# Optimization experiments

Measured on AMD Instinct MI355X. Metric: run time of the kernel, lower is better.

## Reference

```python
import jax, jax.numpy as jnp
import numpy as np

B, T, N, E = 32, 512, 4, 16          # batch, seq_len, num_nodes, num_edges (N*N)
NI, EI = 16, 8                        # node / edge input channels
HN, HE, MH, C = 128, 128, 256, 8      # hidden node/edge, mlp hidden, classes

# complete-graph edge list (matches the src/dst double loop in __init__)
SRC = np.repeat(np.arange(N), N)      # [E]
DST = np.tile(np.arange(N), N)        # [E]
# GCNConv (PyG default) adds self-loops on top of the existing complete graph
# -> adjacency counts: off-diag 1, diag 2; in-degree of every node = N+1.
# symmetric norm deg^-1/2 A deg^-1/2 collapses to A/(N+1). Dense 4x4 matmul
# per graph is the efficient faithful form of the scatter-add here.
NORM_ADJ = (np.ones((N, N), np.float32) + np.eye(N, dtype=np.float32)) / (N + 1)


def lstm(x, Wih, Whh, b):
    """batch_first LSTM, torch gate order (i,f,g,o). x: [Bn,T,D] -> [Bn,T,H]."""
    H = Whh.shape[0]
    xz = x @ Wih + b  # precompute input projection [Bn,T,4H]

    def step(carry, zt):
        h, c = carry
        z = zt + h @ Whh
        i, f, g, o = jnp.split(z, 4, axis=-1)
        c = jax.nn.sigmoid(f) * c + jax.nn.sigmoid(i) * jnp.tanh(g)
        h = jax.nn.sigmoid(o) * jnp.tanh(c)
        return (h, c), h

    init = (jnp.zeros((x.shape[0], H), x.dtype), jnp.zeros((x.shape[0], H), x.dtype))
    _, hs = jax.lax.scan(step, init, jnp.swapaxes(xz, 0, 1))
    return jnp.swapaxes(hs, 0, 1)


def setup_inputs() -> dict:
    key = jax.random.key(0)
    ks = jax.random.split(key, 30)

    def p(k, shape, s=0.05):
        return (jax.random.normal(k, shape, jnp.float32) * s)

    return {
        "x_seq": jax.random.normal(ks[0], (B, T, N, NI), jnp.float32),
        "edge_attr_seq": jax.random.normal(ks[1], (B, T, E, EI), jnp.float32),
        "Wn1": p(ks[2], (NI, HN)), "bn1": p(ks[3], (HN,)),
        "Wn2": p(ks[4], (HN, HN)), "bn2": p(ks[5], (HN,)),
        "We1": p(ks[6], (EI, HE)), "be1": p(ks[7], (HE,)),
        "We2": p(ks[8], (HE, HE)), "be2": p(ks[9], (HE,)),
        "Wg1": p(ks[10], (HN, HN)), "bg1": p(ks[11], (HN,)),
        "Wg2": p(ks[12], (HN, HN)), "bg2": p(ks[13], (HN,)),
        "Wef1": p(ks[14], (HE, HE)), "bef1": p(ks[15], (HE,)),
        "Wef2": p(ks[16], (HE, HE)), "bef2": p(ks[17], (HE,)),
        "Wih_n": p(ks[18], (HN, 4 * HN)), "Whh_n": p(ks[19], (HN, 4 * HN)), "b_n": p(ks[20], (4 * HN,)),
        "Wih_e": p(ks[21], (HE, 4 * HE)), "Whh_e": p(ks[22], (HE, 4 * HE)), "b_e": p(ks[23], (4 * HE,)),
        "Wc1": p(ks[24], (2 * HN + HE, MH)), "bc1": p(ks[25], (MH,)),
        "Wc2": p(ks[26], (MH, C)), "bc2": p(ks[27], (C,)),
    }


def reference(x_seq, edge_attr_seq, Wn1, bn1, Wn2, bn2, We1, be1, We2, be2,
              Wg1, bg1, Wg2, bg2, Wef1, bef1, Wef2, bef2,
              Wih_n, Whh_n, b_n, Wih_e, Whh_e, b_e, Wc1, bc1, Wc2, bc2):
    adj = jnp.asarray(NORM_ADJ)
    # node / edge MLP embeddings
    x = jax.nn.relu(jax.nn.relu(x_seq @ Wn1 + bn1) @ Wn2 + bn2)      # [B,T,N,HN]
    e = jax.nn.relu(jax.nn.relu(edge_attr_seq @ We1 + be1) @ We2 + be2)  # [B,T,E,HE]
    # two GCN layers: normalized-adjacency aggregation per (batch,time) graph
    x = jax.nn.relu(jnp.einsum('ij,btjd->btid', adj, x @ Wg1) + bg1)
    x = jax.nn.relu(jnp.einsum('ij,btjd->btid', adj, x @ Wg2) + bg2)
    # edge FC stack
    e = jax.nn.relu(jax.nn.relu(e @ Wef1 + bef1) @ Wef2 + bef2)
    # LSTMs over time, one sequence per (batch, node) / (batch, edge)
    xn = x.transpose(0, 2, 1, 3).reshape(B * N, T, HN)
    en = e.transpose(0, 2, 1, 3).reshape(B * E, T, HE)
    hn = lstm(xn, Wih_n, Whh_n, b_n).reshape(B, N, T, HN).transpose(0, 2, 1, 3)  # [B,T,N,HN]
    he = lstm(en, Wih_e, Whh_e, b_e).reshape(B, E, T, HE).transpose(0, 2, 1, 3)  # [B,T,E,HE]
    # edge-gather classifier
    src_f = hn[:, :, jnp.asarray(SRC), :]
    dst_f = hn[:, :, jnp.asarray(DST), :]
    feats = jnp.concatenate([src_f, dst_f, he], axis=-1)  # [B,T,E,2HN+HE]
    logits = jax.nn.relu(feats @ Wc1 + bc1) @ Wc2 + bc2   # [B,T,E,C]
    return logits
```

## Files before the change

kernel.cpp:

```cpp
#include <hip/hip_runtime.h>
#include <cstdint>

constexpr int T_  = 512;
constexpr int HN_ = 128;

#define DEVI __device__ __forceinline__

typedef __bf16 bf16x8 __attribute__((ext_vector_type(8)));
typedef __bf16 bf16x4 __attribute__((ext_vector_type(4)));
typedef __bf16 bf16x2 __attribute__((ext_vector_type(2)));
typedef float  f32x4  __attribute__((ext_vector_type(4)));

DEVI float sigf(float x) { return __builtin_amdgcn_rcpf(1.f + __expf(-x)); }
DEVI float tanh_fast(float x) {
  x = fminf(fmaxf(x, -15.f), 15.f);
  return 1.f - 2.f * __builtin_amdgcn_rcpf(1.f + __expf(2.f * x));
}

DEVI void layer128_bf(const __bf16* __restrict__ src, __bf16* __restrict__ dst,
                      bf16x8 w0, bf16x8 w1, bf16x8 w2, bf16x8 w3,
                      float bv, int lm, int lh, int n)
{
  #pragma unroll
  for (int m = 0; m < 4; ++m) {
    const __bf16* sp = &src[(m*16 + lm)*136 + lh*8];
    const bf16x8 a0 = *reinterpret_cast<const bf16x8*>(sp);
    const bf16x8 a1 = *reinterpret_cast<const bf16x8*>(sp + 32);
    const bf16x8 a2 = *reinterpret_cast<const bf16x8*>(sp + 64);
    const bf16x8 a3 = *reinterpret_cast<const bf16x8*>(sp + 96);
    f32x4 acc = { bv, bv, bv, bv };
    acc = __builtin_amdgcn_mfma_f32_16x16x32_bf16(a0, w0, acc, 0, 0, 0);
    acc = __builtin_amdgcn_mfma_f32_16x16x32_bf16(a1, w1, acc, 0, 0, 0);
    acc = __builtin_amdgcn_mfma_f32_16x16x32_bf16(a2, w2, acc, 0, 0, 0);
    acc = __builtin_amdgcn_mfma_f32_16x16x32_bf16(a3, w3, acc, 0, 0, 0);
    #pragma unroll
    for (int r = 0; r < 4; ++r)
      dst[(m*16 + lh*4 + r)*136 + n] = (__bf16)fmaxf(acc[r], 0.f);
  }
}

DEVI void layer128_f32(const __bf16* __restrict__ src, float* __restrict__ dst,
                       bf16x8 w0, bf16x8 w1, bf16x8 w2, bf16x8 w3,
                       float bv, bool relu, int lm, int lh, int n)
{
  #pragma unroll
  for (int m = 0; m < 4; ++m) {
    const __bf16* sp = &src[(m*16 + lm)*136 + lh*8];
    const bf16x8 a0 = *reinterpret_cast<const bf16x8*>(sp);
    const bf16x8 a1 = *reinterpret_cast<const bf16x8*>(sp + 32);
    const bf16x8 a2 = *reinterpret_cast<const bf16x8*>(sp + 64);
    const bf16x8 a3 = *reinterpret_cast<const bf16x8*>(sp + 96);
    f32x4 acc = { bv, bv, bv, bv };
    acc = __builtin_amdgcn_mfma_f32_16x16x32_bf16(a0, w0, acc, 0, 0, 0);
    acc = __builtin_amdgcn_mfma_f32_16x16x32_bf16(a1, w1, acc, 0, 0, 0);
    acc = __builtin_amdgcn_mfma_f32_16x16x32_bf16(a2, w2, acc, 0, 0, 0);
    acc = __builtin_amdgcn_mfma_f32_16x16x32_bf16(a3, w3, acc, 0, 0, 0);
    #pragma unroll
    for (int r = 0; r < 4; ++r)
      dst[(m*16 + lh*4 + r)*132 + n] = relu ? fmaxf(acc[r], 0.f) : acc[r];
  }
}

__global__ __launch_bounds__(512, 4) void node_mlp_mfma_kernel(
    const float* __restrict__ x_seq,
    const float* __restrict__ Wn1, const float* __restrict__ bn1,
    const float* __restrict__ Wn2, const float* __restrict__ bn2,
    const float* __restrict__ Wg1, const float* __restrict__ bg1,
    const float* __restrict__ Wg2, const float* __restrict__ bg2,
    float* __restrict__ xn)
{
  constexpr int P1 = 40;
  __shared__ __align__(16) __bf16 A1[64 * P1];
  __shared__ __align__(16) __bf16 Ab[64 * 136];
  __shared__ __align__(16) __bf16 Bb[64 * 136];
  __shared__ __align__(16) float  Yf[64 * 132];

  const int tid = threadIdx.x;
  const int w = tid >> 6, l = tid & 63, lm = l & 15, lh = l >> 4;
  const int n = w*16 + lm;

  bf16x8 w1, w2[4], w3[4], w4[4];
  const float b1 = bn1[n], b2 = bn2[n];
  #pragma unroll
  for (int j = 0; j < 8; ++j) {
    const int k = lh*8 + j;
    w1[j] = (k < 16) ? (__bf16)Wn1[k*128 + n] : (__bf16)0.f;
  }
  #pragma unroll
  for (int kt = 0; kt < 4; ++kt)
    #pragma unroll
    for (int j = 0; j < 8; ++j) {
      const int k = kt*32 + lh*8 + j;
      w2[kt][j] = (__bf16)Wn2[k*128 + n];
      w3[kt][j] = (__bf16)Wg1[k*128 + n];
      w4[kt][j] = (__bf16)Wg2[k*128 + n];
    }

  for (int i = tid; i < 64 * P1; i += 512) A1[i] = (__bf16)0.f;

  for (int g = blockIdx.x; g < 1024; g += 512) {
    #pragma unroll
    for (int it = 0; it < 2; ++it) {
      const int i = tid + it*512;
      A1[(i >> 4)*P1 + (i & 15)] = (__bf16)x_seq[(size_t)g*1024 + i];
    }
    __syncthreads();
    #pragma unroll
    for (int m = 0; m < 4; ++m) {
      const bf16x8 a = *reinterpret_cast<const bf16x8*>(&A1[(m*16+lm)*P1 + lh*8]);
      f32x4 acc = { b1, b1, b1, b1 };
      acc = __builtin_amdgcn_mfma_f32_16x16x32_bf16(a, w1, acc, 0, 0, 0);
      #pragma unroll
      for (int r = 0; r < 4; ++r)
        Ab[(m*16 + lh*4 + r)*136 + n] = (__bf16)fmaxf(acc[r], 0.f);
    }
    __syncthreads();
    layer128_bf(Ab, Bb, w2[0], w2[1], w2[2], w2[3], b2, lm, lh, n);
    __syncthreads();
    layer128_f32(Bb, Yf, w3[0], w3[1], w3[2], w3[3], 0.f, false, lm, lh, n);
    __syncthreads();
    #pragma unroll
    for (int it = 0; it < 4; ++it) {
      const int idx = tid + it*512;
      const int q = idx >> 7, d = idx & 127;
      const float y0 = Yf[(q*4+0)*132 + d], y1 = Yf[(q*4+1)*132 + d];
      const float y2 = Yf[(q*4+2)*132 + d], y3 = Yf[(q*4+3)*132 + d];
      const float s = y0 + y1 + y2 + y3;
      const float bv = bg1[d];
      Ab[(q*4+0)*136 + d] = (__bf16)fmaxf((s + y0)*0.2f + bv, 0.f);
      Ab[(q*4+1)*136 + d] = (__bf16)fmaxf((s + y1)*0.2f + bv, 0.f);
      Ab[(q*4+2)*136 + d] = (__bf16)fmaxf((s + y2)*0.2f + bv, 0.f);
      Ab[(q*4+3)*136 + d] = (__bf16)fmaxf((s + y3)*0.2f + bv, 0.f);
    }
    __syncthreads();
    layer128_f32(Ab, Yf, w4[0], w4[1], w4[2], w4[3], 0.f, false, lm, lh, n);
    __syncthreads();
    #pragma unroll
    for (int it = 0; it < 4; ++it) {
      const int idx = tid + it*512;
      const int q = idx >> 7, d = idx & 127;
      const int bt = g*16 + q, bb = bt >> 9, tt = bt & 511;
      const float y0 = Yf[(q*4+0)*132 + d], y1 = Yf[(q*4+1)*132 + d];
      const float y2 = Yf[(q*4+2)*132 + d], y3 = Yf[(q*4+3)*132 + d];
      const float s = y0 + y1 + y2 + y3;
      const float bv = bg2[d];
      xn[((size_t)(bb*4+0)*T_ + tt)*HN_ + d] = fmaxf((s + y0)*0.2f + bv, 0.f);
      xn[((size_t)(bb*4+1)*T_ + tt)*HN_ + d] = fmaxf((s + y1)*0.2f + bv, 0.f);
      xn[((size_t)(bb*4+2)*T_ + tt)*HN_ + d] = fmaxf((s + y2)*0.2f + bv, 0.f);
      xn[((size_t)(bb*4+3)*T_ + tt)*HN_ + d] = fmaxf((s + y3)*0.2f + bv, 0.f);
    }
    __syncthreads();
  }
}

__global__ __launch_bounds__(512, 4) void edge_mlp_mfma_kernel(
    const float* __restrict__ ea,
    const float* __restrict__ We1, const float* __restrict__ be1,
    const float* __restrict__ We2, const float* __restrict__ be2,
    const float* __restrict__ Wef1, const float* __restrict__ bef1,
    const float* __restrict__ Wef2, const float* __restrict__ bef2,
    float* __restrict__ en)
{
  constexpr int P1 = 40;
  __shared__ __align__(16) __bf16 A1[64 * P1];
  __shared__ __align__(16) __bf16 Ab[64 * 136];
  __shared__ __align__(16) __bf16 Bb[64 * 136];
  __shared__ __align__(16) float  Of[64 * 132];

  const int tid = threadIdx.x;
  const int w = tid >> 6, l = tid & 63, lm = l & 15, lh = l >> 4;
  const int n = w*16 + lm;

  bf16x8 w1, w2[4], w3[4], w4[4];
  const float b1 = be1[n], b2 = be2[n], b3 = bef1[n], b4 = bef2[n];
  #pragma unroll
  for (int j = 0; j < 8; ++j) {
    const int k = lh*8 + j;
    w1[j] = (k < 8) ? (__bf16)We1[k*128 + n] : (__bf16)0.f;
  }
  #pragma unroll
  for (int kt = 0; kt < 4; ++kt)
    #pragma unroll
    for (int j = 0; j < 8; ++j) {
      const int k = kt*32 + lh*8 + j;
      w2[kt][j] = (__bf16)We2[k*128 + n];
      w3[kt][j] = (__bf16)Wef1[k*128 + n];
      w4[kt][j] = (__bf16)Wef2[k*128 + n];
    }

  for (int i = tid; i < 64 * P1; i += 512) A1[i] = (__bf16)0.f;

  for (int g = blockIdx.x; g < 4096; g += 512) {
    A1[(tid >> 3)*P1 + (tid & 7)] = (__bf16)ea[(size_t)g*512 + tid];
    __syncthreads();
    #pragma unroll
    for (int m = 0; m < 4; ++m) {
      const bf16x8 a = *reinterpret_cast<const bf16x8*>(&A1[(m*16+lm)*P1 + lh*8]);
      f32x4 acc = { b1, b1, b1, b1 };
      acc = __builtin_amdgcn_mfma_f32_16x16x32_bf16(a, w1, acc, 0, 0, 0);
      #pragma unroll
      for (int r = 0; r < 4; ++r)
        Ab[(m*16 + lh*4 + r)*136 + n] = (__bf16)fmaxf(acc[r], 0.f);
    }
    __syncthreads();
    layer128_bf(Ab, Bb, w2[0], w2[1], w2[2], w2[3], b2, lm, lh, n);
    __syncthreads();
    layer128_bf(Bb, Ab, w3[0], w3[1], w3[2], w3[3], b3, lm, lh, n);
    __syncthreads();
    layer128_f32(Ab, Of, w4[0], w4[1], w4[2], w4[3], b4, true, lm, lh, n);
    __syncthreads();
    #pragma unroll
    for (int i = 0; i < 4; ++i) {
      const int fi = tid + i*512;
      const int row = fi >> 5, c4 = fi & 31;
      const int q = row >> 4, e = row & 15;
      const int bt = g*4 + q, bb = bt >> 9, tt = bt & 511;
      const float4 v = *reinterpret_cast<const float4*>(&Of[row*132 + c4*4]);
      *reinterpret_cast<float4*>(
          &en[((size_t)(bb*16+e)*T_ + tt)*HN_ + c4*4]) = v;
    }
    __syncthreads();
  }
}

__global__ __launch_bounds__(512, 1) void lstm_mfma_kernel(
    const float* __restrict__ Wih_n, const float* __restrict__ Whh_n,
    const float* __restrict__ b_n,
    const float* __restrict__ Wih_e, const float* __restrict__ Whh_e,
    const float* __restrict__ b_e,
    float* __restrict__ xn, float* __restrict__ en)
{
  constexpr int XROW = 2064;
  constexpr int HROW = 144;
  constexpr int SPAD = 2056;
  __shared__ __align__(16) __bf16 x_c[8 * XROW];
  __shared__ __align__(16) __bf16 x_zero[XROW];
  __shared__ __align__(16) __bf16 h_bf[8 * HROW];
  __shared__ __align__(16) __bf16 h_zero[HROW];
  __shared__ __align__(16) float  h_hist[8 * SPAD];

  const bool is_node = (int)blockIdx.x < 16;
  const int  bidx    = is_node ? blockIdx.x : ((int)blockIdx.x - 16);
  const float* __restrict__ Wih  = is_node ? Wih_n : Wih_e;
  const float* __restrict__ Whh  = is_node ? Whh_n : Whh_e;
  const float* __restrict__ bias = is_node ? b_n   : b_e;
  float* __restrict__ xh = (is_node ? xn : en) + (size_t)bidx * 8 * (T_ * HN_);

  const int tid = threadIdx.x;
  const int w   = tid >> 6;
  const int l   = tid & 63;
  const int lm  = l & 15;
  const int lh  = l >> 4;

  bf16x8 wih_f[4][4], whh_f[4][4];
  f32x4  bias_v[4];
  #pragma unroll
  for (int nt = 0; nt < 4; ++nt) {
    const int g0 = nt*128 + w*16;
    bias_v[nt] = *reinterpret_cast<const f32x4*>(&bias[g0 + lh*4]);
    #pragma unroll
    for (int kt = 0; kt < 4; ++kt) {
      #pragma unroll
      for (int j = 0; j < 8; ++j) {
        const int k = kt*32 + lh*8 + j;
        wih_f[nt][kt][j] = (__bf16)Wih[k*512 + g0 + lm];
        whh_f[nt][kt][j] = (__bf16)Whh[k*512 + g0 + lm];
      }
    }
  }

  for (int i = tid; i < XROW; i += 512) x_zero[i] = (__bf16)0.f;
  for (int i = tid; i < 8 * HROW; i += 512) h_bf[i] = (__bf16)0.f;
  if (tid < HROW) h_zero[tid] = (__bf16)0.f;

  const __bf16* __restrict__ xrow = (lm < 8) ? &x_c[lm * XROW] : x_zero;
  const __bf16* __restrict__ hrow = (lm < 8) ? &h_bf[lm * HROW] : h_zero;

  const bool hi_half = lm >= 8;
  const int  s  = lm & 7;
  const int  dl = w*16 + lh*4 + (hi_half ? 2 : 0);
  float c0 = 0.f, c1 = 0.f;

  for (int t = 0; t < T_; ++t) {
    if ((t & 15) == 0) {
      if (t) {
        #pragma unroll
        for (int i = 0; i < 8; ++i) {
          const int fi = tid + i*512;
          const int sq = fi >> 9, rem = fi & 511;
          const int tl = rem >> 5, k = (rem & 31)*4;
          const float4 v = *reinterpret_cast<const float4*>(
              &h_hist[sq*SPAD + tl*128 + k]);
          *reinterpret_cast<float4*>(
              &xh[(size_t)sq*(T_*HN_) + (size_t)(t-16+tl)*HN_ + k]) = v;
        }
      }
      #pragma unroll
      for (int i = 0; i < 8; ++i) {
        const int f4  = (tid + i*512) * 4;
        const int sq  = f4 >> 11;
        const int rem = f4 & 2047;
        const float4 v = *reinterpret_cast<const float4*>(
            &xh[(size_t)sq*(T_*HN_) + (size_t)t*HN_ + rem]);
        bf16x4 pk;
        pk[0] = (__bf16)v.x; pk[1] = (__bf16)v.y;
        pk[2] = (__bf16)v.z; pk[3] = (__bf16)v.w;
        *reinterpret_cast<bf16x4*>(&x_c[sq*XROW + rem]) = pk;
      }
      __syncthreads();
    }
    const int tl = t & 15;

    bf16x8 bx[4], bh[4];
    #pragma unroll
    for (int kt = 0; kt < 4; ++kt) {
      bx[kt] = *reinterpret_cast<const bf16x8*>(&xrow[tl*128 + kt*32 + lh*8]);
      bh[kt] = *reinterpret_cast<const bf16x8*>(&hrow[kt*32 + lh*8]);
    }

    f32x4 accs[4];
    #pragma unroll
    for (int nt = 0; nt < 4; ++nt) {
      f32x4 acc = bias_v[nt];
      #pragma unroll
      for (int kt = 0; kt < 4; ++kt) {
        acc = __builtin_amdgcn_mfma_f32_16x16x32_bf16(wih_f[nt][kt], bx[kt], acc, 0, 0, 0);
        acc = __builtin_amdgcn_mfma_f32_16x16x32_bf16(whh_f[nt][kt], bh[kt], acc, 0, 0, 0);
      }
      accs[nt] = acc;
    }

    float z0[4], z1[4];
    #pragma unroll
    for (int nt = 0; nt < 4; ++nt) {
      const float a2 = __shfl_up(accs[nt][2], 8u, 16);
      const float a3 = __shfl_up(accs[nt][3], 8u, 16);
      z0[nt] = hi_half ? a2 : accs[nt][0];
      z1[nt] = hi_half ? a3 : accs[nt][1];
    }
    c0 = sigf(z0[1]) * c0 + sigf(z0[0]) * tanh_fast(z0[2]);
    const float h0 = sigf(z0[3]) * tanh_fast(c0);
    c1 = sigf(z1[1]) * c1 + sigf(z1[0]) * tanh_fast(z1[2]);
    const float h1 = sigf(z1[3]) * tanh_fast(c1);

    bf16x2 hb; hb[0] = (__bf16)h0; hb[1] = (__bf16)h1;
    *reinterpret_cast<bf16x2*>(&h_bf[s*HROW + dl]) = hb;
    float2 ho; ho.x = h0; ho.y = h1;
    *reinterpret_cast<float2*>(&h_hist[s*SPAD + tl*128 + dl]) = ho;
    __syncthreads();
  }
  #pragma unroll
  for (int i = 0; i < 8; ++i) {
    const int fi = tid + i*512;
    const int sq = fi >> 9, rem = fi & 511;
    const int tl = rem >> 5, k = (rem & 31)*4;
    const float4 v = *reinterpret_cast<const float4*>(
        &h_hist[sq*SPAD + tl*128 + k]);
    *reinterpret_cast<float4*>(
        &xh[(size_t)sq*(T_*HN_) + (size_t)(T_-16+tl)*HN_ + k]) = v;
  }
}

__global__ __launch_bounds__(512, 1) void classifier_mfma_kernel(
    const float* __restrict__ hn, const float* __restrict__ he,
    const float* __restrict__ Wc1, const float* __restrict__ bc1,
    const float* __restrict__ Wc2, const float* __restrict__ bc2,
    float* __restrict__ out)
{
  constexpr int HP = 136;
  constexpr int DP = 264;
  __shared__ __align__(16) __bf16 hn_l[32 * HP];
  __shared__ __align__(16) __bf16 he_l[128 * HP];
  __shared__ __align__(16) __bf16 hid_l[128 * DP];

  const int tid = threadIdx.x;
  const int w   = tid >> 6;
  const int l   = tid & 63;
  const int lm  = l & 15;
  const int lh  = l >> 4;

  bf16x8 wb[2][12];
  float  bcol[2];
  #pragma unroll
  for (int jt = 0; jt < 2; ++jt) {
    const int j = w*32 + jt*16 + lm;
    bcol[jt] = bc1[j];
    #pragma unroll
    for (int kt = 0; kt < 12; ++kt)
      #pragma unroll
      for (int i = 0; i < 8; ++i)
        wb[jt][kt][i] = (__bf16)Wc1[(kt*32 + lh*8 + i)*256 + j];
  }
  bf16x8 wc2f[8];
  const float bc2v = (lm < 8) ? bc2[lm] : 0.f;
  #pragma unroll
  for (int kt = 0; kt < 8; ++kt)
    #pragma unroll
    for (int i = 0; i < 8; ++i)
      wc2f[kt][i] = (lm < 8) ? (__bf16)Wc2[(kt*32 + lh*8 + i)*8 + lm] : (__bf16)0.f;

  for (int g = blockIdx.x; g < 2048; g += 256) {
    const int b  = g >> 6;
    const int t0 = (g & 63) * 8;

    for (int i = tid; i < 4096; i += 512) {
      const int f4 = i * 4;
      const int e  = f4 >> 10;
      const int rem = f4 & 1023;
      const int tt = rem >> 7;
      const int k  = rem & 127;
      const float4 v = *reinterpret_cast<const float4*>(
          &he[((size_t)(b*16+e)*T_ + t0 + tt)*HN_ + k]);
      __bf16* p = &he_l[(tt*16 + e)*HP + k];
      p[0]=(__bf16)v.x; p[1]=(__bf16)v.y; p[2]=(__bf16)v.z; p[3]=(__bf16)v.w;
    }
    for (int i = tid; i < 1024; i += 512) {
      const int f4 = i * 4;
      const int n  = f4 >> 10;
      const int rem = f4 & 1023;
      const int tt = rem >> 7;
      const int k  = rem & 127;
      const float4 v = *reinterpret_cast<const float4*>(
          &hn[((size_t)(b*4+n)*T_ + t0 + tt)*HN_ + k]);
      __bf16* p = &hn_l[(tt*4 + n)*HP + k];
      p[0]=(__bf16)v.x; p[1]=(__bf16)v.y; p[2]=(__bf16)v.z; p[3]=(__bf16)v.w;
    }
    __syncthreads();

    for (int tt = 0; tt < 8; ++tt) {
      bf16x8 af[12];
      #pragma unroll
      for (int kt = 0; kt < 4; ++kt)
        af[kt] = *reinterpret_cast<const bf16x8*>(
            &hn_l[(tt*4 + (lm>>2))*HP + kt*32 + lh*8]);
      #pragma unroll
      for (int kt = 0; kt < 4; ++kt)
        af[4+kt] = *reinterpret_cast<const bf16x8*>(
            &hn_l[(tt*4 + (lm&3))*HP + kt*32 + lh*8]);
      #pragma unroll
      for (int kt = 0; kt < 4; ++kt)
        af[8+kt] = *reinterpret_cast<const bf16x8*>(
            &he_l[(tt*16 + lm)*HP + kt*32 + lh*8]);
      #pragma unroll
      for (int jt = 0; jt < 2; ++jt) {
        f32x4 acc = { bcol[jt], bcol[jt], bcol[jt], bcol[jt] };
        #pragma unroll
        for (int kt = 0; kt < 12; ++kt)
          acc = __builtin_amdgcn_mfma_f32_16x16x32_bf16(af[kt], wb[jt][kt], acc, 0, 0, 0);
        #pragma unroll
        for (int r = 0; r < 4; ++r)
          hid_l[(tt*16 + lh*4 + r)*DP + (w*2 + jt)*16 + lm] = (__bf16)fmaxf(acc[r], 0.f);
      }
    }
    __syncthreads();

    {
      const int tt = w;
      f32x4 acc = { bc2v, bc2v, bc2v, bc2v };
      #pragma unroll
      for (int kt = 0; kt < 8; ++kt) {
        const bf16x8 a = *reinterpret_cast<const bf16x8*>(
            &hid_l[(tt*16 + lm)*DP + kt*32 + lh*8]);
        acc = __builtin_amdgcn_mfma_f32_16x16x32_bf16(a, wc2f[kt], acc, 0, 0, 0);
      }
      if (lm < 8) {
        const size_t bt = (size_t)b*T_ + t0 + tt;
        #pragma unroll
        for (int r = 0; r < 4; ++r)
          out[(bt*16 + lh*4 + r)*8 + lm] = acc[r];
      }
    }
    __syncthreads();
  }
}

extern "C" void kernel_launch(void* const* d_in, const int* in_sizes, int n_in,
                              void* d_out, int out_size, void* d_ws, size_t ws_size,
                              hipStream_t stream) {
  (void)in_sizes; (void)n_in; (void)out_size; (void)ws_size;
  const float* x_seq = (const float*)d_in[0];
  const float* ea    = (const float*)d_in[1];
  const float* Wn1 = (const float*)d_in[2];
  const float* bn1 = (const float*)d_in[3];
  const float* Wn2 = (const float*)d_in[4];
  const float* bn2 = (const float*)d_in[5];
  const float* We1 = (const float*)d_in[6];
  const float* be1 = (const float*)d_in[7];
  const float* We2 = (const float*)d_in[8];
  const float* be2 = (const float*)d_in[9];
  const float* Wg1 = (const float*)d_in[10];
  const float* bg1 = (const float*)d_in[11];
  const float* Wg2 = (const float*)d_in[12];
  const float* bg2 = (const float*)d_in[13];
  const float* Wef1 = (const float*)d_in[14];
  const float* bef1 = (const float*)d_in[15];
  const float* Wef2 = (const float*)d_in[16];
  const float* bef2 = (const float*)d_in[17];
  const float* Wih_n = (const float*)d_in[18];
  const float* Whh_n = (const float*)d_in[19];
  const float* b_n   = (const float*)d_in[20];
  const float* Wih_e = (const float*)d_in[21];
  const float* Whh_e = (const float*)d_in[22];
  const float* b_e   = (const float*)d_in[23];
  const float* Wc1 = (const float*)d_in[24];
  const float* bc1 = (const float*)d_in[25];
  const float* Wc2 = (const float*)d_in[26];
  const float* bc2 = (const float*)d_in[27];

  float* xn = (float*)d_ws;
  float* en = xn + (size_t)128 * T_ * HN_;
  float* out = (float*)d_out;

  node_mlp_mfma_kernel<<<512, 512, 0, stream>>>(x_seq, Wn1, bn1, Wn2, bn2,
                                                Wg1, bg1, Wg2, bg2, xn);
  edge_mlp_mfma_kernel<<<512, 512, 0, stream>>>(ea, We1, be1, We2, be2,
                                                Wef1, bef1, Wef2, bef2, en);
  lstm_mfma_kernel<<<80, 512, 0, stream>>>(Wih_n, Whh_n, b_n,
                                           Wih_e, Whh_e, b_e, xn, en);
  classifier_mfma_kernel<<<256, 512, 0, stream>>>(xn, en, Wc1, bc1, Wc2, bc2, out);
}
```

Before: 776.3 us.

## Swizzle LSTM shared-memory layouts, prefetch x fragments, split MFMA accumulators

Replaces padded shared-memory rows in the recurrent LSTM kernel with XOR-swizzled layouts for x_c, h_bf and h_hist to avoid LDS bank conflicts without padding. Prefetches the next timestep's input fragments after the MFMAs so that load leaves the serial critical path. Splits the input and recurrent MFMA chains into two independent accumulators to shorten the dependency chain, and swaps shfl_up for a ds_swizzle xor. The risk is added index arithmetic and a possible mismatch in the swizzle mapping.

New measurement: 827.1 us. 1.07x slower.

```diff
diff --git a/kernel.cpp b/kernel.cpp
--- a/kernel.cpp
+++ b/kernel.cpp
@@ -15,6 +15,9 @@
 DEVI float tanh_fast(float x) {
   x = fminf(fmaxf(x, -15.f), 15.f);
   return 1.f - 2.f * __builtin_amdgcn_rcpf(1.f + __expf(2.f * x));
+}
+DEVI float swz_xor8(float x) {
+  return __int_as_float(__builtin_amdgcn_ds_swizzle(__float_as_int(x), 0x201F));
 }
 
 DEVI void layer128_bf(const __bf16* __restrict__ src, __bf16* __restrict__ dst,
@@ -230,14 +233,11 @@
     const float* __restrict__ b_e,
     float* __restrict__ xn, float* __restrict__ en)
 {
-  constexpr int XROW = 2064;
-  constexpr int HROW = 144;
-  constexpr int SPAD = 2056;
-  __shared__ __align__(16) __bf16 x_c[8 * XROW];
-  __shared__ __align__(16) __bf16 x_zero[XROW];
-  __shared__ __align__(16) __bf16 h_bf[8 * HROW];
-  __shared__ __align__(16) __bf16 h_zero[HROW];
-  __shared__ __align__(16) float  h_hist[8 * SPAD];
+  __shared__ __align__(16) __bf16 x_c[8 * 2048];
+  __shared__ __align__(16) __bf16 x_zero[2048];
+  __shared__ __align__(16) __bf16 h_bf[8 * 128];
+  __shared__ __align__(16) __bf16 h_zero[128];
+  __shared__ __align__(16) float  h_hist[8 * 2048];
 
   const bool is_node = (int)blockIdx.x < 16;
   const int  bidx    = is_node ? blockIdx.x : ((int)blockIdx.x - 16);
@@ -269,72 +269,85 @@
     }
   }
 
-  for (int i = tid; i < XROW; i += 512) x_zero[i] = (__bf16)0.f;
-  for (int i = tid; i < 8 * HROW; i += 512) h_bf[i] = (__bf16)0.f;
-  if (tid < HROW) h_zero[tid] = (__bf16)0.f;
-
-  const __bf16* __restrict__ xrow = (lm < 8) ? &x_c[lm * XROW] : x_zero;
-  const __bf16* __restrict__ hrow = (lm < 8) ? &h_bf[lm * HROW] : h_zero;
+  for (int i = tid; i < 2048; i += 512) x_zero[i] = (__bf16)0.f;
+  for (int i = tid; i < 8 * 128; i += 512) h_bf[i] = (__bf16)0.f;
+  if (tid < 128) h_zero[tid] = (__bf16)0.f;
+
+  const int swz = (lm < 8) ? ((lm & 7) << 4) : 0;
+  const __bf16* __restrict__ xrow = (lm < 8) ? &x_c[lm * 2048] : x_zero;
+  const __bf16* __restrict__ hrow = (lm < 8) ? &h_bf[lm * 128] : h_zero;
+  int foff[4];
+  #pragma unroll
+  for (int kt = 0; kt < 4; ++kt)
+    foff[kt] = ((kt*64 + lh*16) ^ swz) >> 1;
 
   const bool hi_half = lm >= 8;
   const int  s  = lm & 7;
-  const int  dl = w*16 + lh*4 + (hi_half ? 2 : 0);
+  const int hb_unit = (2*w + (lh >> 1)) ^ s;
+  const int hb_idx  = s*128 + (((hb_unit << 4) + 8*(lh & 1) + (hi_half ? 4 : 0)) >> 1);
+  const int hh_col  = (w*4 + lh) ^ s;
+  const int hh_base = s*2048 + hh_col*4 + (hi_half ? 2 : 0);
   float c0 = 0.f, c1 = 0.f;
 
+  bf16x8 bx[4];
   for (int t = 0; t < T_; ++t) {
-    if ((t & 15) == 0) {
+    const int tl = t & 15;
+    if (tl == 0) {
       if (t) {
         #pragma unroll
         for (int i = 0; i < 8; ++i) {
-          const int fi = tid + i*512;
-          const int sq = fi >> 9, rem = fi & 511;
-          const int tl = rem >> 5, k = (rem & 31)*4;
+          const int tl2 = tid >> 5, u = tid & 31;
           const float4 v = *reinterpret_cast<const float4*>(
-              &h_hist[sq*SPAD + tl*128 + k]);
+              &h_hist[i*2048 + (tid ^ (i & 7))*4]);
           *reinterpret_cast<float4*>(
-              &xh[(size_t)sq*(T_*HN_) + (size_t)(t-16+tl)*HN_ + k]) = v;
+              &xh[(size_t)i*(T_*HN_) + (size_t)(t-16+tl2)*HN_ + u*4]) = v;
         }
       }
       #pragma unroll
       for (int i = 0; i < 8; ++i) {
-        const int f4  = (tid + i*512) * 4;
-        const int sq  = f4 >> 11;
-        const int rem = f4 & 2047;
         const float4 v = *reinterpret_cast<const float4*>(
-            &xh[(size_t)sq*(T_*HN_) + (size_t)t*HN_ + rem]);
+            &xh[(size_t)i*(T_*HN_) + (size_t)t*HN_ + tid*4]);
         bf16x4 pk;
         pk[0] = (__bf16)v.x; pk[1] = (__bf16)v.y;
         pk[2] = (__bf16)v.z; pk[3] = (__bf16)v.w;
-        *reinterpret_cast<bf16x4*>(&x_c[sq*XROW + rem]) = pk;
+        *reinterpret_cast<bf16x4*>(
+            &x_c[i*2048 + (((tid >> 1) ^ (i & 7)) << 3) + (tid & 1)*4]) = pk;
       }
       __syncthreads();
-    }
-    const int tl = t & 15;
-
-    bf16x8 bx[4], bh[4];
-    #pragma unroll
-    for (int kt = 0; kt < 4; ++kt) {
-      bx[kt] = *reinterpret_cast<const bf16x8*>(&xrow[tl*128 + kt*32 + lh*8]);
-      bh[kt] = *reinterpret_cast<const bf16x8*>(&hrow[kt*32 + lh*8]);
-    }
+      #pragma unroll
+      for (int kt = 0; kt < 4; ++kt)
+        bx[kt] = *reinterpret_cast<const bf16x8*>(&xrow[foff[kt]]);
+    }
+
+    bf16x8 bh[4];
+    #pragma unroll
+    for (int kt = 0; kt < 4; ++kt)
+      bh[kt] = *reinterpret_cast<const bf16x8*>(&hrow[foff[kt]]);
 
     f32x4 accs[4];
     #pragma unroll
     for (int nt = 0; nt < 4; ++nt) {
-      f32x4 acc = bias_v[nt];
+      f32x4 aA = bias_v[nt];
+      f32x4 aB = { 0.f, 0.f, 0.f, 0.f };
       #pragma unroll
       for (int kt = 0; kt < 4; ++kt) {
-        acc = __builtin_amdgcn_mfma_f32_16x16x32_bf16(wih_f[nt][kt], bx[kt], acc, 0, 0, 0);
-        acc = __builtin_amdgcn_mfma_f32_16x16x32_bf16(whh_f[nt][kt], bh[kt], acc, 0, 0, 0);
-      }
-      accs[nt] = acc;
+        aA = __builtin_amdgcn_mfma_f32_16x16x32_bf16(wih_f[nt][kt], bx[kt], aA, 0, 0, 0);
+        aB = __builtin_amdgcn_mfma_f32_16x16x32_bf16(whh_f[nt][kt], bh[kt], aB, 0, 0, 0);
+      }
+      accs[nt] = aA + aB;
+    }
+
+    if (tl != 15) {
+      #pragma unroll
+      for (int kt = 0; kt < 4; ++kt)
+        bx[kt] = *reinterpret_cast<const bf16x8*>(&xrow[(tl+1)*128 + foff[kt]]);
     }
 
     float z0[4], z1[4];
     #pragma unroll
     for (int nt = 0; nt < 4; ++nt) {
-      const float a2 = __shfl_up(accs[nt][2], 8u, 16);
-      const float a3 = __shfl_up(accs[nt][3], 8u, 16);
+      const float a2 = swz_xor8(accs[nt][2]);
+      const float a3 = swz_xor8(accs[nt][3]);
       z0[nt] = hi_half ? a2 : accs[nt][0];
       z1[nt] = hi_half ? a3 : accs[nt][1];
     }
@@ -344,20 +357,18 @@
     const float h1 = sigf(z1[3]) * tanh_fast(c1);
 
     bf16x2 hb; hb[0] = (__bf16)h0; hb[1] = (__bf16)h1;
-    *reinterpret_cast<bf16x2*>(&h_bf[s*HROW + dl]) = hb;
+    *reinterpret_cast<bf16x2*>(&h_bf[hb_idx]) = hb;
     float2 ho; ho.x = h0; ho.y = h1;
-    *reinterpret_cast<float2*>(&h_hist[s*SPAD + tl*128 + dl]) = ho;
+    *reinterpret_cast<float2*>(&h_hist[hh_base + tl*128]) = ho;
     __syncthreads();
   }
   #pragma unroll
   for (int i = 0; i < 8; ++i) {
-    const int fi = tid + i*512;
-    const int sq = fi >> 9, rem = fi & 511;
-    const int tl = rem >> 5, k = (rem & 31)*4;
+    const int tl2 = tid >> 5, u = tid & 31;
     const float4 v = *reinterpret_cast<const float4*>(
-        &h_hist[sq*SPAD + tl*128 + k]);
+        &h_hist[i*2048 + (tid ^ (i & 7))*4]);
     *reinterpret_cast<float4*>(
-        &xh[(size_t)sq*(T_*HN_) + (size_t)(T_-16+tl)*HN_ + k]) = v;
+        &xh[(size_t)i*(T_*HN_) + (size_t)(T_-16+tl2)*HN_ + u*4]) = v;
   }
 }
 
```
